# Optimization experiments

Hardware: AMD Instinct MI355X
Metric: run time of the kernel (lower is better)

## Reference

```python
import jax, jax.numpy as jnp
import numpy as np

FS = 30.0   # sampling_rate from __init__
B, T = 32768, 2048


def setup_inputs() -> dict:
    key = jax.random.key(0)
    x = jax.random.normal(key, (B, T), dtype=jnp.float32)
    return {"x": x}


def _trapz_slice(pairs, a, b):
    # trapz of s[a:b] with dx=1/FS, given precomputed trapezoid pairs
    # pairs[i] = 0.5*(s[i]+s[i+1]); integral sums i in [a, b-2]. Empty slice -> 0.
    i = jnp.arange(pairs.shape[0])
    m = ((i >= a) & (i <= b - 2)).astype(pairs.dtype)
    return jnp.sum(pairs * m) / FS


def _features(s):
    n = s.shape[0]
    # ---- time-domain: [max, ptp, var(ddof=1), std(ddof=1)] ----
    mx = jnp.max(s)
    ptp = mx - jnp.min(s)
    var = jnp.var(s, ddof=1)
    std = jnp.sqrt(var)
    # ---- frequency-domain: mean |FFT| ----
    mean_amp = jnp.mean(jnp.abs(jnp.fft.fft(s)))
    # ---- peak / valley detection on interior points (index i+1 in signal) ----
    l, m_, r = s[:-2], s[1:-1], s[2:]
    peak_m = (l < m_) & (m_ > r)
    val_m = (l > m_) & (m_ < r)
    n_peaks = jnp.sum(peak_m)
    n_vals = jnp.sum(val_m)
    pos = jnp.arange(n - 2)
    p0 = jnp.argmax(peak_m) + 1                       # peaks[0]
    v0 = jnp.argmax(val_m) + 1                        # valleys[0]
    v1 = jnp.argmax(val_m & (pos > (v0 - 1))) + 1     # valleys[1]
    vlast = (n - 3) - jnp.argmax(val_m[::-1]) + 1     # valleys[-1]
    # ---- iPPG features ----
    pairs = 0.5 * (s[:-1] + s[1:])
    PA = _trapz_slice(pairs, v0, vlast)
    A2 = _trapz_slice(pairs, p0, v1)
    PH = s[p0] - s[v0]
    A1 = _trapz_slice(pairs, v0, p0)
    # half-height width between valleys[0] and peaks[0]
    half = 0.5 * (s[p0] + s[v0])
    idx = jnp.arange(n)
    lm = (idx >= v0) & (idx < p0) & (s >= half)
    left_i = jnp.where(jnp.any(lm), jnp.argmax(lm), v0)
    rm = (idx <= p0) & (idx > v0) & (s >= half)
    right_i = jnp.where(jnp.any(rm), (n - 1) - jnp.argmax(rm[::-1]), p0)
    PWHH = (right_i - left_i).astype(s.dtype) / FS
    ippg = jnp.stack([PA, A2, PH, A1, PWHH])
    ippg = jnp.where((n_peaks >= 1) & (n_vals >= 2), ippg, jnp.zeros(5, s.dtype))
    return jnp.concatenate([jnp.stack([mx, ptp, var, std, mean_amp]), ippg])


def reference(x):
    return jax.vmap(_features)(x)  # [B, 10]
```

## Files before the change

### kernel.cpp

```cpp
#include <hip/hip_runtime.h>
#include <math.h>

#define NTH 256
#define PAD64(i) ((i) + ((i) >> 6))

#define CMUL(vr, vi, c, s) { float _tr = (vr)*(c) - (vi)*(s); (vi) = (vr)*(s) + (vi)*(c); (vr) = _tr; }

#define FFT4(r0,i0,r1,i1,r2,i2,r3,i3) {                     \
    float _acr=(r0)+(r2), _aci=(i0)+(i2);                   \
    float _scr=(r0)-(r2), _sci=(i0)-(i2);                   \
    float _bdr=(r1)+(r3), _bdi=(i1)+(i3);                   \
    float _sdr=(r1)-(r3), _sdi=(i1)-(i3);                   \
    (r0)=_acr+_bdr; (i0)=_aci+_bdi;                         \
    (r1)=_scr+_sdi; (i1)=_sci-_sdr;                         \
    (r2)=_acr-_bdr; (i2)=_aci-_bdi;                         \
    (r3)=_scr-_sdi; (i3)=_sci+_sdr; }

__device__ __forceinline__ void fft16(float* xr, float* xi) {
    const float C1 = 0.92387953251128675613f;
    const float S1 = 0.38268343236508977172f;
    const float R2 = 0.70710678118654752440f;
#pragma unroll
    for (int q = 0; q < 4; ++q)
        FFT4(xr[q], xi[q], xr[4+q], xi[4+q], xr[8+q], xi[8+q], xr[12+q], xi[12+q]);
    CMUL(xr[5],  xi[5],   C1, -S1);
    CMUL(xr[9],  xi[9],   R2, -R2);
    CMUL(xr[13], xi[13],  S1, -C1);
    CMUL(xr[6],  xi[6],   R2, -R2);
    { float t = xr[10]; xr[10] = xi[10]; xi[10] = -t; }
    CMUL(xr[14], xi[14], -R2, -R2);
    CMUL(xr[7],  xi[7],   S1, -C1);
    CMUL(xr[11], xi[11], -R2, -R2);
    CMUL(xr[15], xi[15], -C1,  S1);
#pragma unroll
    for (int s = 0; s < 4; ++s)
        FFT4(xr[4*s], xi[4*s], xr[4*s+1], xi[4*s+1], xr[4*s+2], xi[4*s+2], xr[4*s+3], xi[4*s+3]);
}

__global__ __launch_bounds__(NTH, 4)
void feat_kernel(const float* __restrict__ gx, float* __restrict__ gout) {
    const int tid = threadIdx.x;
    const int wv  = tid >> 6;
    const int ln  = tid & 63;
    const int row = blockIdx.x * 4 + wv;
    const float* xrow = gx + (size_t)row * 2048;

    __shared__ float ZRs[4][1040], ZIs[4][1040];
    float* Zr = ZRs[wv];
    float* Zi = ZIs[wv];

    const float4* x4 = (const float4*)xrow;
#pragma unroll
    for (int t = 0; t < 8; ++t) {
        float4 u = x4[ln + 64 * t];
        int c = 2 * (ln + 64 * t);
        int a = PAD64(c);
        Zr[a]     = u.x; Zi[a]     = u.y;
        Zr[a + 1] = u.z; Zi[a + 1] = u.w;
    }

    float r[32];
    {
        int base = PAD64(16 * ln);
#pragma unroll
        for (int j = 0; j < 16; ++j) {
            r[2*j]   = Zr[base + j];
            r[2*j+1] = Zi[base + j];
        }
    }

    float vmax = r[0], vmin = r[0], vsum = r[0];
#pragma unroll
    for (int e = 1; e < 32; ++e) {
        vmax = fmaxf(vmax, r[e]); vmin = fminf(vmin, r[e]); vsum += r[e];
    }
#pragma unroll
    for (int o = 1; o < 64; o <<= 1) {
        vmax = fmaxf(vmax, __shfl_xor(vmax, o, 64));
        vmin = fminf(vmin, __shfl_xor(vmin, o, 64));
        vsum += __shfl_xor(vsum, o, 64);
    }
    float mx = vmax, mn = vmin, mean = vsum * (1.0f / 2048.0f);

    float ss = 0.0f;
#pragma unroll
    for (int e = 0; e < 32; ++e) { float d = r[e] - mean; ss += d * d; }
#pragma unroll
    for (int o = 1; o < 64; o <<= 1) ss += __shfl_xor(ss, o, 64);
    float var = ss * (1.0f / 2047.0f);
    float sd  = sqrtf(var);

    float lN = __shfl_up(r[31], 1, 64);
    float rN = __shfl_down(r[0], 1, 64);
    unsigned pm = 0, vm = 0;
#pragma unroll
    for (int m = 0; m < 32; ++m) {
        int p = 32 * ln + m;
        float l  = (m == 0)  ? lN : r[m - 1];
        float mm = r[m];
        float rt = (m == 31) ? rN : r[m + 1];
        bool ok = (p >= 1) && (p <= 2046);
        pm |= (unsigned)(ok && (l < mm) && (mm > rt)) << m;
        vm |= (unsigned)(ok && (l > mm) && (mm < rt)) << m;
    }
    int cp = __popc(pm), cv = __popc(vm);
    int mp = pm ? 32 * ln + __ffs(pm) - 1 : (1 << 30);
    int mv = vm ? 32 * ln + __ffs(vm) - 1 : (1 << 30);
    int Mv = vm ? 32 * ln + 31 - __clz(vm) : -1;
#pragma unroll
    for (int o = 1; o < 64; o <<= 1) {
        cp += __shfl_xor(cp, o, 64);
        cv += __shfl_xor(cv, o, 64);
        mp = min(mp, __shfl_xor(mp, o, 64));
        mv = min(mv, __shfl_xor(mv, o, 64));
        Mv = max(Mv, __shfl_xor(Mv, o, 64));
    }
    const int n_peaks = cp, n_vals = cv, p0 = mp, v0 = mv, vlast = Mv;

    float PA = 0.0f, A2f = 0.0f, PH = 0.0f, A1f = 0.0f, PW = 0.0f;
    if (n_peaks >= 1 && n_vals >= 2) {
        int lo = v0 - 32 * ln;
        unsigned sel = (lo < 0) ? 0xFFFFFFFFu : ((lo >= 31) ? 0u : (0xFFFFFFFFu << (lo + 1)));
        unsigned m2 = vm & sel;
        int mv2 = m2 ? 32 * ln + __ffs(m2) - 1 : (1 << 30);
#pragma unroll
        for (int o = 1; o < 64; o <<= 1) mv2 = min(mv2, __shfl_xor(mv2, o, 64));
        int v1 = mv2;

        float sp0 = (p0 & 1) ? Zi[PAD64(p0 >> 1)] : Zr[PAD64(p0 >> 1)];
        float sv0 = (v0 & 1) ? Zi[PAD64(v0 >> 1)] : Zr[PAD64(v0 >> 1)];
        PH = sp0 - sv0;
        float half = 0.5f * (sp0 + sv0);

        float aPA = 0.0f, aA2 = 0.0f, aA1 = 0.0f;
        int li = 1 << 30, ri = -1;
#pragma unroll
        for (int m = 0; m < 32; ++m) {
            int i = 32 * ln + m;
            float si = r[m];
            if (i < 2047) {
                float nx = (m == 31) ? rN : r[m + 1];
                float pr = 0.5f * (si + nx);
                if (i >= v0 && i <= vlast - 2) aPA += pr;
                if (i >= p0 && i <= v1 - 2)    aA2 += pr;
                if (i >= v0 && i <= p0 - 2)    aA1 += pr;
            }
            if (si >= half) {
                if (i >= v0 && i < p0)  li = min(li, i);
                if (i > v0 && i <= p0)  ri = max(ri, i);
            }
        }
#pragma unroll
        for (int o = 1; o < 64; o <<= 1) {
            aPA += __shfl_xor(aPA, o, 64);
            aA2 += __shfl_xor(aA2, o, 64);
            aA1 += __shfl_xor(aA1, o, 64);
            li = min(li, __shfl_xor(li, o, 64));
            ri = max(ri, __shfl_xor(ri, o, 64));
        }
        PA  = aPA * (1.0f / 30.0f);
        A2f = aA2 * (1.0f / 30.0f);
        A1f = aA1 * (1.0f / 30.0f);
        if (li == (1 << 30)) li = v0;
        if (ri < 0)          ri = p0;
        PW = (float)(ri - li) * (1.0f / 30.0f);
    }

    float ar[16], ai[16];
#pragma unroll
    for (int n2 = 0; n2 < 16; ++n2) {
        ar[n2] = Zr[ln + 65 * n2];
        ai[n2] = Zi[ln + 65 * n2];
    }
    fft16(ar, ai);
    {
        int wbase = PAD64(16 * ln);
        float fl = (float)ln;
#pragma unroll
        for (int idx = 0; idx < 16; ++idx) {
            int k2 = (idx >> 2) + 4 * (idx & 3);
            if (k2 > 0) {
                float ang = fl * (float)k2 * (-6.2831853071795864769e0f / 1024.0f);
                float c = __cosf(ang), s = __sinf(ang);
                CMUL(ar[idx], ai[idx], c, s);
            }
            Zr[wbase + k2] = ar[idx];
            Zi[wbase + k2] = ai[idx];
        }
    }
    const int al  = ln & 3;
    const int k2r = ln >> 2;
    {
        int base = 16 * al + k2r;
#pragma unroll
        for (int b = 0; b < 16; ++b) {
            ar[b] = Zr[base + 65 * b];
            ai[b] = Zi[base + 65 * b];
        }
    }
    fft16(ar, ai);
    {
        float fa = (float)al;
#pragma unroll
        for (int idx = 0; idx < 16; ++idx) {
            int j = (idx >> 2) + 4 * (idx & 3);
            if (j > 0) {
                float ang = fa * (float)j * (-6.2831853071795864769e0f / 64.0f);
                float c = __cosf(ang), s = __sinf(ang);
                CMUL(ar[idx], ai[idx], c, s);
            }
        }
    }
    {
        const bool hi = (al & 2) != 0;
        const bool b0 = (al & 1) != 0;
        const int g = ((al & 1) << 1) | (al >> 1);
        int fbase = k2r + 260 * g;
#pragma unroll
        for (int idx = 0; idx < 16; ++idx) {
            int j = (idx >> 2) + 4 * (idx & 3);
            float tr = __shfl_xor(ar[idx], 2, 64);
            float ti = __shfl_xor(ai[idx], 2, 64);
            float vr = hi ? (tr - ar[idx]) : (ar[idx] + tr);
            float vi = hi ? (ti - ai[idx]) : (ai[idx] + ti);
            float sr = __shfl_xor(vr, 1, 64);
            float si = __shfl_xor(vi, 1, 64);
            float Xr, Xi;
            if (!b0) { Xr = hi ? (vr + si) : (vr + sr); Xi = hi ? (vi - sr) : (vi + si); }
            else     { Xr = hi ? (sr - vi) : (sr - vr); Xi = hi ? (si + vr) : (si - vi); }
            Zr[fbase + 16 * j + (j >> 2)] = Xr;
            Zi[fbase + 16 * j + (j >> 2)] = Xi;
        }
    }

    float amp = 0.0f;
#pragma unroll
    for (int t = 0; t < 9; ++t) {
        int k = ln + 64 * t;
        if (k <= 512) {
            int m = (1024 - k) & 1023;
            float zr = Zr[ln + 65 * t], zi = Zi[ln + 65 * t];
            int ma = PAD64(m);
            float mr = Zr[ma], mi = Zi[ma];
            float Er = 0.5f * (zr + mr), Ei = 0.5f * (zi - mi);
            float Or = 0.5f * (zi + mi), Oi = 0.5f * (mr - zr);
            float ang = (float)k * (-3.14159265358979323846f / 1024.0f);
            float c = __cosf(ang), s = __sinf(ang);
            float Pr = Or * c - Oi * s, Pi = Or * s + Oi * c;
            float x1r = Er + Pr, x1i = Ei + Pi;
            float x2r = Er - Pr, x2i = Ei - Pi;
            float w = (k == 0 || k == 512) ? 1.0f : 2.0f;
            amp += w * (__builtin_amdgcn_sqrtf(x1r * x1r + x1i * x1i) +
                        __builtin_amdgcn_sqrtf(x2r * x2r + x2i * x2i));
        }
    }
#pragma unroll
    for (int o = 1; o < 64; o <<= 1) amp += __shfl_xor(amp, o, 64);
    float mean_amp = amp * (1.0f / 2048.0f);

    if (ln == 0) {
        float* o = gout + (size_t)row * 10;
        o[0] = mx;
        o[1] = mx - mn;
        o[2] = var;
        o[3] = sd;
        o[4] = mean_amp;
        o[5] = PA;
        o[6] = A2f;
        o[7] = PH;
        o[8] = A1f;
        o[9] = PW;
    }
}

extern "C" void kernel_launch(void* const* d_in, const int* in_sizes, int n_in,
                              void* d_out, int out_size, void* d_ws, size_t ws_size,
                              hipStream_t stream) {
    (void)d_ws; (void)ws_size; (void)n_in; (void)out_size;
    const float* x = (const float*)d_in[0];
    float* out = (float*)d_out;
    int rows = in_sizes[0] / 2048;
    feat_kernel<<<dim3(rows / 4), dim3(NTH), 0, stream>>>(x, out);
}
```

Measured before the change: 396.9 us.

## Swizzle LDS layout, fuse variance pass, use recurrence twiddles and bitmask peaks

Replaces padded shared-memory indexing with XOR-swizzled addresses, which shrinks LDS per wave and raises the occupancy hint to 5. Variance now comes from a single sum/sum-of-squares pass. Peak and valley detection is built from comparison bitmasks, and the trapezoid integrals are taken from prefix-style sums with endpoint corrections. FFT twiddles come from angle-doubling recurrences instead of repeated sin/cos calls. The risks are reduced numerical accuracy from the one-pass variance and the accumulated twiddle recurrences.

```diff
diff --git a/kernel.cpp b/kernel.cpp
--- a/kernel.cpp
+++ b/kernel.cpp
@@ -2,7 +2,6 @@
 #include <math.h>
 
 #define NTH 256
-#define PAD64(i) ((i) + ((i) >> 6))
 
 #define CMUL(vr, vi, c, s) { float _tr = (vr)*(c) - (vi)*(s); (vi) = (vr)*(s) + (vi)*(c); (vr) = _tr; }
 
@@ -37,7 +36,7 @@
         FFT4(xr[4*s], xi[4*s], xr[4*s+1], xi[4*s+1], xr[4*s+2], xi[4*s+2], xr[4*s+3], xi[4*s+3]);
 }
 
-__global__ __launch_bounds__(NTH, 4)
+__global__ __launch_bounds__(NTH, 5)
 void feat_kernel(const float* __restrict__ gx, float* __restrict__ gout) {
     const int tid = threadIdx.x;
     const int wv  = tid >> 6;
@@ -45,77 +44,81 @@
     const int row = blockIdx.x * 4 + wv;
     const float* xrow = gx + (size_t)row * 2048;
 
-    __shared__ float ZRs[4][1040], ZIs[4][1040];
+    __shared__ float ZRs[4][1024], ZIs[4][1024];
     float* Zr = ZRs[wv];
     float* Zi = ZIs[wv];
 
+    const int al  = ln & 3;
+    const int k2r = ln >> 2;
+    const int b5  = ln >> 5;
+
     const float4* x4 = (const float4*)xrow;
 #pragma unroll
     for (int t = 0; t < 8; ++t) {
         float4 u = x4[ln + 64 * t];
-        int c = 2 * (ln + 64 * t);
-        int a = PAD64(c);
-        Zr[a]     = u.x; Zi[a]     = u.y;
-        Zr[a + 1] = u.z; Zi[a + 1] = u.w;
+        int c  = 2 * ln + 128 * t;
+        int a0 = c ^ (2 * t + b5);
+        int a1 = a0 ^ 1;
+        Zr[a0] = u.x; Zi[a0] = u.y;
+        Zr[a1] = u.z; Zi[a1] = u.w;
     }
 
     float r[32];
     {
-        int base = PAD64(16 * ln);
+        int base = 16 * ln;
 #pragma unroll
         for (int j = 0; j < 16; ++j) {
-            r[2*j]   = Zr[base + j];
-            r[2*j+1] = Zi[base + j];
-        }
-    }
-
-    float vmax = r[0], vmin = r[0], vsum = r[0];
-#pragma unroll
-    for (int e = 1; e < 32; ++e) {
-        vmax = fmaxf(vmax, r[e]); vmin = fminf(vmin, r[e]); vsum += r[e];
+            int a = base + (j ^ k2r);
+            r[2*j]   = Zr[a];
+            r[2*j+1] = Zi[a];
+        }
+    }
+
+    float vmax = r[0], vmin = r[0], vsum = 0.0f, vsq = 0.0f;
+#pragma unroll
+    for (int e = 0; e < 32; ++e) {
+        vmax = fmaxf(vmax, r[e]); vmin = fminf(vmin, r[e]);
+        vsum += r[e]; vsq = fmaf(r[e], r[e], vsq);
     }
 #pragma unroll
     for (int o = 1; o < 64; o <<= 1) {
         vmax = fmaxf(vmax, __shfl_xor(vmax, o, 64));
         vmin = fminf(vmin, __shfl_xor(vmin, o, 64));
         vsum += __shfl_xor(vsum, o, 64);
+        vsq  += __shfl_xor(vsq,  o, 64);
     }
     float mx = vmax, mn = vmin, mean = vsum * (1.0f / 2048.0f);
-
-    float ss = 0.0f;
-#pragma unroll
-    for (int e = 0; e < 32; ++e) { float d = r[e] - mean; ss += d * d; }
-#pragma unroll
-    for (int o = 1; o < 64; o <<= 1) ss += __shfl_xor(ss, o, 64);
-    float var = ss * (1.0f / 2047.0f);
+    float var = (vsq - vsum * mean) * (1.0f / 2047.0f);
     float sd  = sqrtf(var);
 
     float lN = __shfl_up(r[31], 1, 64);
-    float rN = __shfl_down(r[0], 1, 64);
-    unsigned pm = 0, vm = 0;
+    unsigned aw = 0, bw = 0;
 #pragma unroll
     for (int m = 0; m < 32; ++m) {
-        int p = 32 * ln + m;
-        float l  = (m == 0)  ? lN : r[m - 1];
-        float mm = r[m];
-        float rt = (m == 31) ? rN : r[m + 1];
-        bool ok = (p >= 1) && (p <= 2046);
-        pm |= (unsigned)(ok && (l < mm) && (mm > rt)) << m;
-        vm |= (unsigned)(ok && (l > mm) && (mm < rt)) << m;
-    }
-    int cp = __popc(pm), cv = __popc(vm);
+        float l = (m == 0) ? lN : r[m - 1];
+        float c = r[m];
+        aw |= (unsigned)(l < c) << m;
+        bw |= (unsigned)(l > c) << m;
+    }
+    unsigned an = __shfl_down(aw, 1, 64) & 1u;
+    unsigned bn = __shfl_down(bw, 1, 64) & 1u;
+    unsigned pm = aw & ((bw >> 1) | (bn << 31));
+    unsigned vm = bw & ((aw >> 1) | (an << 31));
+    if (ln == 0)  { pm &= ~1u; vm &= ~1u; }
+    if (ln == 63) { pm &= 0x7FFFFFFFu; vm &= 0x7FFFFFFFu; }
+
+    int pk = __popc(pm) | (__popc(vm) << 12);
     int mp = pm ? 32 * ln + __ffs(pm) - 1 : (1 << 30);
     int mv = vm ? 32 * ln + __ffs(vm) - 1 : (1 << 30);
     int Mv = vm ? 32 * ln + 31 - __clz(vm) : -1;
 #pragma unroll
     for (int o = 1; o < 64; o <<= 1) {
-        cp += __shfl_xor(cp, o, 64);
-        cv += __shfl_xor(cv, o, 64);
+        pk += __shfl_xor(pk, o, 64);
         mp = min(mp, __shfl_xor(mp, o, 64));
         mv = min(mv, __shfl_xor(mv, o, 64));
         Mv = max(Mv, __shfl_xor(Mv, o, 64));
     }
-    const int n_peaks = cp, n_vals = cv, p0 = mp, v0 = mv, vlast = Mv;
+    const int n_peaks = pk & 0xFFF, n_vals = pk >> 12, p0 = mp, v0 = mv, vlast = Mv;
 
     float PA = 0.0f, A2f = 0.0f, PH = 0.0f, A1f = 0.0f, PW = 0.0f;
     if (n_peaks >= 1 && n_vals >= 2) {
@@ -125,97 +128,111 @@
         int mv2 = m2 ? 32 * ln + __ffs(m2) - 1 : (1 << 30);
 #pragma unroll
         for (int o = 1; o < 64; o <<= 1) mv2 = min(mv2, __shfl_xor(mv2, o, 64));
-        int v1 = mv2;
-
-        float sp0 = (p0 & 1) ? Zi[PAD64(p0 >> 1)] : Zr[PAD64(p0 >> 1)];
-        float sv0 = (v0 & 1) ? Zi[PAD64(v0 >> 1)] : Zr[PAD64(v0 >> 1)];
-        PH = sp0 - sv0;
-        float half = 0.5f * (sp0 + sv0);
-
-        float aPA = 0.0f, aA2 = 0.0f, aA1 = 0.0f;
+        const int v1 = mv2;
+
+        auto sAt = [&](int p) -> float {
+            int e = p >> 1;
+            int a = e ^ (e >> 6);
+            return (p & 1) ? Zi[a] : Zr[a];
+        };
+        float s_v0  = sAt(v0), s_p0 = sAt(p0);
+        float s_pm1 = sAt(p0 - 1), s_v1m1 = sAt(v1 - 1), s_vLm1 = sAt(vlast - 1);
+        PH = s_p0 - s_v0;
+        float half = 0.5f * (s_p0 + s_v0);
+
+        float S1 = 0.0f, S2 = 0.0f, S3 = 0.0f;
         int li = 1 << 30, ri = -1;
 #pragma unroll
         for (int m = 0; m < 32; ++m) {
             int i = 32 * ln + m;
             float si = r[m];
-            if (i < 2047) {
-                float nx = (m == 31) ? rN : r[m + 1];
-                float pr = 0.5f * (si + nx);
-                if (i >= v0 && i <= vlast - 2) aPA += pr;
-                if (i >= p0 && i <= v1 - 2)    aA2 += pr;
-                if (i >= v0 && i <= p0 - 2)    aA1 += pr;
+            bool geV0 = (i >= v0), geP0 = (i >= p0);
+            if (geV0 && !geP0)  S1 += si;
+            if (geP0 && i < v1) S2 += si;
+            if (geV0 && i < vlast) S3 += si;
+            if (si >= half) {
+                if (geV0 && !geP0)     li = min(li, i);
+                if (i > v0 && i <= p0) ri = max(ri, i);
             }
-            if (si >= half) {
-                if (i >= v0 && i < p0)  li = min(li, i);
-                if (i > v0 && i <= p0)  ri = max(ri, i);
-            }
         }
 #pragma unroll
         for (int o = 1; o < 64; o <<= 1) {
-            aPA += __shfl_xor(aPA, o, 64);
-            aA2 += __shfl_xor(aA2, o, 64);
-            aA1 += __shfl_xor(aA1, o, 64);
+            S1 += __shfl_xor(S1, o, 64);
+            S2 += __shfl_xor(S2, o, 64);
+            S3 += __shfl_xor(S3, o, 64);
             li = min(li, __shfl_xor(li, o, 64));
             ri = max(ri, __shfl_xor(ri, o, 64));
         }
-        PA  = aPA * (1.0f / 30.0f);
-        A2f = aA2 * (1.0f / 30.0f);
-        A1f = aA1 * (1.0f / 30.0f);
+        PA  = (S3 - 0.5f * (s_v0 + s_vLm1)) * (1.0f / 30.0f);
+        A2f = (v1 > p0) ? (S2 - 0.5f * (s_p0 + s_v1m1)) * (1.0f / 30.0f) : 0.0f;
+        A1f = (p0 > v0) ? (S1 - 0.5f * (s_v0 + s_pm1)) * (1.0f / 30.0f) : 0.0f;
         if (li == (1 << 30)) li = v0;
         if (ri < 0)          ri = p0;
         PW = (float)(ri - li) * (1.0f / 30.0f);
     }
 
+    float s0, c0;
+    __sincosf((float)ln * (-3.14159265358979323846f / 1024.0f), &s0, &c0);
+
     float ar[16], ai[16];
 #pragma unroll
     for (int n2 = 0; n2 < 16; ++n2) {
-        ar[n2] = Zr[ln + 65 * n2];
-        ai[n2] = Zi[ln + 65 * n2];
+        int a = (ln ^ n2) + 64 * n2;
+        ar[n2] = Zr[a];
+        ai[n2] = Zi[a];
     }
     fft16(ar, ai);
     {
-        int wbase = PAD64(16 * ln);
-        float fl = (float)ln;
-#pragma unroll
-        for (int idx = 0; idx < 16; ++idx) {
-            int k2 = (idx >> 2) + 4 * (idx & 3);
-            if (k2 > 0) {
-                float ang = fl * (float)k2 * (-6.2831853071795864769e0f / 1024.0f);
-                float c = __cosf(ang), s = __sinf(ang);
-                CMUL(ar[idx], ai[idx], c, s);
-            }
-            Zr[wbase + k2] = ar[idx];
-            Zi[wbase + k2] = ai[idx];
-        }
-    }
-    const int al  = ln & 3;
-    const int k2r = ln >> 2;
-    {
-        int base = 16 * al + k2r;
+        const float cb = c0 * c0 - s0 * s0;
+        const float sb = 2.0f * c0 * s0;
+        int wb = 16 * ln;
+        Zr[wb + k2r] = ar[0];
+        Zi[wb + k2r] = ai[0];
+        float cc = cb, ss = sb;
+#pragma unroll
+        for (int k2 = 1; k2 < 16; ++k2) {
+            const int idx = (k2 >> 2) + 4 * (k2 & 3);
+            CMUL(ar[idx], ai[idx], cc, ss);
+            int a = wb + (k2 ^ k2r);
+            Zr[a] = ar[idx];
+            Zi[a] = ai[idx];
+            float nc = cc * cb - ss * sb;
+            ss = cc * sb + ss * cb;
+            cc = nc;
+        }
+    }
+    {
+        int cbase = 16 * al;
 #pragma unroll
         for (int b = 0; b < 16; ++b) {
-            ar[b] = Zr[base + 65 * b];
-            ai[b] = Zi[base + 65 * b];
+            int a = cbase + (k2r ^ b) + 64 * b;
+            ar[b] = Zr[a];
+            ai[b] = Zi[a];
         }
     }
     fft16(ar, ai);
     {
-        float fa = (float)al;
-#pragma unroll
-        for (int idx = 0; idx < 16; ++idx) {
-            int j = (idx >> 2) + 4 * (idx & 3);
-            if (j > 0) {
-                float ang = fa * (float)j * (-6.2831853071795864769e0f / 64.0f);
-                float c = __cosf(ang), s = __sinf(ang);
-                CMUL(ar[idx], ai[idx], c, s);
-            }
+        float cA = (al & 1) ? 0.99518472667219688624f : 1.0f;
+        float sA = (al & 1) ? -0.09801714032956060199f : 0.0f;
+        float cB = (al & 1) ? 0.95694033573220886494f : 0.98078528040323044913f;
+        float sB = (al & 1) ? -0.29028467725446236764f : -0.19509032201612826785f;
+        float c1 = (al & 2) ? cB : cA;
+        float s1 = (al & 2) ? sB : sA;
+        float cc = c1, ss = s1;
+#pragma unroll
+        for (int j = 1; j < 16; ++j) {
+            const int idx = (j >> 2) + 4 * (j & 3);
+            CMUL(ar[idx], ai[idx], cc, ss);
+            float nc = cc * c1 - ss * s1;
+            ss = cc * s1 + ss * c1;
+            cc = nc;
         }
     }
     {
         const bool hi = (al & 2) != 0;
         const bool b0 = (al & 1) != 0;
         const int g = ((al & 1) << 1) | (al >> 1);
-        int fbase = k2r + 260 * g;
+        int fbase = k2r + 256 * g;
 #pragma unroll
         for (int idx = 0; idx < 16; ++idx) {
             int j = (idx >> 2) + 4 * (idx & 3);
@@ -228,30 +245,39 @@
             float Xr, Xi;
             if (!b0) { Xr = hi ? (vr + si) : (vr + sr); Xi = hi ? (vi - sr) : (vi + si); }
             else     { Xr = hi ? (sr - vi) : (sr - vr); Xi = hi ? (si + vr) : (si - vi); }
-            Zr[fbase + 16 * j + (j >> 2)] = Xr;
-            Zi[fbase + 16 * j + (j >> 2)] = Xi;
+            Zr[fbase + 16 * j] = Xr;
+            Zi[fbase + 16 * j] = Xi;
         }
     }
 
     float amp = 0.0f;
-#pragma unroll
-    for (int t = 0; t < 9; ++t) {
-        int k = ln + 64 * t;
-        if (k <= 512) {
+    {
+        float rc = c0, rs = s0;
+        const float C16 = 0.98078528040323044913f, S16 = 0.19509032201612826785f;
+#pragma unroll
+        for (int t = 0; t < 8; ++t) {
+            int k = ln + 64 * t;
             int m = (1024 - k) & 1023;
-            float zr = Zr[ln + 65 * t], zi = Zi[ln + 65 * t];
-            int ma = PAD64(m);
-            float mr = Zr[ma], mi = Zi[ma];
+            float zr = Zr[k], zi = Zi[k];
+            float mr = Zr[m], mi = Zi[m];
             float Er = 0.5f * (zr + mr), Ei = 0.5f * (zi - mi);
             float Or = 0.5f * (zi + mi), Oi = 0.5f * (mr - zr);
-            float ang = (float)k * (-3.14159265358979323846f / 1024.0f);
-            float c = __cosf(ang), s = __sinf(ang);
-            float Pr = Or * c - Oi * s, Pi = Or * s + Oi * c;
+            float Pr = Or * rc - Oi * rs, Pi = Or * rs + Oi * rc;
             float x1r = Er + Pr, x1i = Ei + Pi;
             float x2r = Er - Pr, x2i = Ei - Pi;
-            float w = (k == 0 || k == 512) ? 1.0f : 2.0f;
-            amp += w * (__builtin_amdgcn_sqrtf(x1r * x1r + x1i * x1i) +
-                        __builtin_amdgcn_sqrtf(x2r * x2r + x2i * x2i));
+            amp += 2.0f * (__builtin_amdgcn_sqrtf(x1r * x1r + x1i * x1i) +
+                           __builtin_amdgcn_sqrtf(x2r * x2r + x2i * x2i));
+            float nr = rc * C16 + rs * S16;
+            rs = rs * C16 - rc * S16;
+            rc = nr;
+        }
+        {
+            float zr0 = Zr[0], zi0 = Zi[0];
+            float q1 = zr0 + zi0, q2 = zr0 - zi0;
+            float corr0 = __builtin_amdgcn_sqrtf(q1 * q1) + __builtin_amdgcn_sqrtf(q2 * q2);
+            float zr5 = Zr[512], zi5 = Zi[512];
+            float c512 = 2.0f * __builtin_amdgcn_sqrtf(zr5 * zr5 + zi5 * zi5);
+            amp += (ln == 0) ? (c512 - corr0) : 0.0f;
         }
     }
 #pragma unroll
```

Result: slower. 595.1 us (+49.9%).
